# Kernel tuning notes

Measured on AMD Instinct MI355X. Metric: run time of the kernel, lower is better.

Reference implementation:

```python
import jax, jax.numpy as jnp
import numpy as np

OUT_SIZE = (7, 7, 7)
SPATIAL_SCALE = 1.0
SAMPLING_RATIO = 2
ALIGNED = True


def setup_inputs() -> dict:
    key = jax.random.key(0)
    kf, kc1, kc2 = jax.random.split(key, 3)
    B, C, D, H, W = 2, 128, 16, 64, 64
    N = 64
    features = jax.random.normal(kf, (B, C, D, H, W), dtype=jnp.float32)
    # Build valid boxes (z1,y1,x1,z2,y2,x2) inside the feature volume.
    dims = jnp.array([D, H, W], dtype=jnp.float32)
    lo = jax.random.uniform(kc1, (B, N, 3)) * dims * 0.6
    ext = 2.0 + jax.random.uniform(kc2, (B, N, 3)) * dims * 0.35
    hi = jnp.minimum(lo + ext, dims - 1.0)
    rois = jnp.concatenate([lo, hi], axis=-1).astype(jnp.float32)  # [B,N,6]
    return {"features": features, "rois": rois}


def _trilinear_sample(feat, z, y, x):
    # feat: [C,D,H,W]; z,y,x: [N,Pd,Ph,Pw] pixel coords (align_corners=False,
    # zero padding: out-of-bounds corners contribute 0).
    C, D, H, W = feat.shape
    z0f, y0f, x0f = jnp.floor(z), jnp.floor(y), jnp.floor(x)
    lz, ly, lx = z - z0f, y - y0f, x - x0f
    z0 = z0f.astype(jnp.int32)
    y0 = y0f.astype(jnp.int32)
    x0 = x0f.astype(jnp.int32)
    feat_flat = feat.reshape(C, -1)  # [C, D*H*W]

    def corner(zi, yi, xi, w):
        valid = ((zi >= 0) & (zi < D) & (yi >= 0) & (yi < H) & (xi >= 0) & (xi < W))
        idx = (jnp.clip(zi, 0, D - 1) * H + jnp.clip(yi, 0, H - 1)) * W + jnp.clip(xi, 0, W - 1)
        vals = jnp.take(feat_flat, idx.reshape(-1), axis=1).reshape((C,) + idx.shape)
        return vals * (w * valid.astype(w.dtype))[None]

    out = corner(z0, y0, x0, (1 - lz) * (1 - ly) * (1 - lx))
    out = out + corner(z0, y0, x0 + 1, (1 - lz) * (1 - ly) * lx)
    out = out + corner(z0, y0 + 1, x0, (1 - lz) * ly * (1 - lx))
    out = out + corner(z0, y0 + 1, x0 + 1, (1 - lz) * ly * lx)
    out = out + corner(z0 + 1, y0, x0, lz * (1 - ly) * (1 - lx))
    out = out + corner(z0 + 1, y0, x0 + 1, lz * (1 - ly) * lx)
    out = out + corner(z0 + 1, y0 + 1, x0, lz * ly * (1 - lx))
    out = out + corner(z0 + 1, y0 + 1, x0 + 1, lz * ly * lx)
    return out  # [C,N,Pd,Ph,Pw]


def _roi_align_3d(features, rois):
    B, C, D, H, W = features.shape
    od, oh, ow = OUT_SIZE
    s = SAMPLING_RATIO if SAMPLING_RATIO > 0 else 1
    dt = features.dtype
    d_step = (jnp.arange(od * s, dtype=dt) + 0.5) / s
    h_step = (jnp.arange(oh * s, dtype=dt) + 0.5) / s
    w_step = (jnp.arange(ow * s, dtype=dt) + 0.5) / s

    def per_batch(feat, roi):  # feat [C,D,H,W], roi [N,6]
        roi = roi * SPATIAL_SCALE
        if ALIGNED:
            roi = roi - 0.5
        z1, y1, x1, z2, y2, x2 = (roi[:, i] for i in range(6))
        bd = jnp.maximum(z2 - z1, 1e-6) / od
        bh = jnp.maximum(y2 - y1, 1e-6) / oh
        bw = jnp.maximum(x2 - x1, 1e-6) / ow
        zg = z1[:, None] + d_step[None, :] * bd[:, None]  # [N, od*s]
        yg = y1[:, None] + h_step[None, :] * bh[:, None]  # [N, oh*s]
        xg = x1[:, None] + w_step[None, :] * bw[:, None]  # [N, ow*s]
        z, y, x = jnp.broadcast_arrays(zg[:, :, None, None], yg[:, None, :, None], xg[:, None, None, :])
        sam = _trilinear_sample(feat, z, y, x)  # [C,N,od*s,oh*s,ow*s]
        N = roi.shape[0]
        sam = sam.reshape(C, N, od, s, oh, s, ow, s).mean(axis=(3, 5, 7))
        return sam.transpose(1, 0, 2, 3, 4)  # [N,C,od,oh,ow]

    return jax.vmap(per_batch)(features, rois)  # [B,N,C,od,oh,ow]


def reference(features, rois):
    return _roi_align_3d(features, rois)
```

## Files before the change

### kernel.cpp

```cpp
#include <hip/hip_runtime.h>

constexpr int Bc = 2, Nc = 64, Cc = 128, Dc = 16, Hc = 64, Wc = 64;
constexpr int OD = 7, OH = 7, OW = 7;
constexpr int CELLS = OD * OH * OW;
constexpr int DHW = Dc * Hc * Wc, HW = Hc * Wc;
constexpr int MAXZ = 10, MAXY = 25, MAXX = 25;
constexpr int SUBSZ = MAXZ * MAXY * (MAXX + 1);

typedef __fp16 h2 __attribute__((ext_vector_type(2)));

__device__ inline unsigned pk_f16(float a, float b) {
    return __builtin_bit_cast(unsigned, __builtin_amdgcn_cvt_pkrtz(a, b));
}

__device__ inline float fdot2(unsigned a, unsigned b, float c) {
#if __has_builtin(__builtin_amdgcn_fdot2)
    return __builtin_amdgcn_fdot2(__builtin_bit_cast(h2, a),
                                  __builtin_bit_cast(h2, b), c, false);
#else
    h2 ha = __builtin_bit_cast(h2, a);
    h2 hb = __builtin_bit_cast(h2, b);
    return fmaf((float)ha.x, (float)hb.x, fmaf((float)ha.y, (float)hb.y, c));
#endif
}

__global__ __launch_bounds__(384) void roialign3d_v11(
    const float* __restrict__ feat, const float* __restrict__ rois,
    float* __restrict__ out)
{
    __shared__ unsigned sub[SUBSZ + 2];
    __shared__ int2     tzp[14], typ[14];
    __shared__ float2   wzp[14], wyp[14];
    __shared__ int      txo[14];
    __shared__ unsigned wxh[14];

    const int blk = blockIdx.x;
    const int cp  = blk & 63;
    const int n   = (blk >> 6) & 63;
    const int b   = blk >> 12;
    const int tid = threadIdx.x;

    const float* rp = rois + (size_t)(b * Nc + n) * 6;
    float r1a[3] = {rp[0] - 0.5f, rp[1] - 0.5f, rp[2] - 0.5f};
    float r2a[3] = {rp[3] - 0.5f, rp[4] - 0.5f, rp[5] - 0.5f};
    const int dims[3] = {Dc, Hc, Wc};
    const int maxn[3] = {MAXZ, MAXY, MAXX};

    float bs[3]; int lo[3], ncnt[3];
    #pragma unroll
    for (int a = 0; a < 3; ++a) {
        bs[a] = fmaxf(r2a[a] - r1a[a], 1e-6f) * (1.0f / 7.0f);
        float smin = r1a[a] + 0.25f * bs[a];
        float smax = r1a[a] + 6.75f * bs[a];
        int l = max(0, (int)floorf(smin));
        int h = min(dims[a] - 1, (int)floorf(smax) + 1);
        lo[a] = l;
        ncnt[a] = min(h - l + 1, maxn[a]);
    }
    const int zn = ncnt[0], yn = ncnt[1], xn = ncnt[2];
    const int xnp = xn | 1;
    const int rows = zn * yn;
    const int zstride = yn * xnp;

    if (tid < 42) {
        int a = tid / 14, m = tid - a * 14;
        float v = r1a[a] + ((float)m + 0.5f) * 0.5f * bs[a];
        float f = floorf(v);
        float l = v - f;
        int i0 = (int)f;
        int d  = dims[a];
        float w0 = (i0 >= 0 && i0 < d) ? 1.0f - l : 0.0f;
        float w1 = (i0 + 1 < d) ? l : 0.0f;
        if (a == 0) {
            int c0 = min(max(i0 - lo[0], 0), zn - 1);
            int c1 = min(max(i0 + 1 - lo[0], 0), zn - 1);
            tzp[m] = make_int2(c0, c1);
            wzp[m] = make_float2(w0, w1);
        } else if (a == 1) {
            int c0 = min(max(i0 - lo[1], 0), yn - 1);
            int c1 = min(max(i0 + 1 - lo[1], 0), yn - 1);
            typ[m] = make_int2(c0 * xnp, c1 * xnp);
            wyp[m] = make_float2(w0, w1);
        } else {
            int c0 = min(max(i0 - lo[2], -1), xn - 1);
            txo[m] = c0;
            wxh[m] = pk_f16(w0, w1);
        }
    }
    if (tid == 64) sub[0] = 0;
    if (tid == 65) sub[1 + rows * xnp] = 0;

    const int c0ch = cp * 2;
    const float* fb = feat + ((size_t)b * Cc + c0ch) * DHW;
    const unsigned m32x = 0xFFFFFFFFu / (unsigned)xnp + 1u;
    const unsigned m32y = 0xFFFFFFFFu / (unsigned)yn + 1u;
    const int gz = lo[0] * HW + lo[1] * Wc + lo[2];
    const int total = rows * xnp;
    for (int p = tid; p < total; p += 384) {
        int row = (int)__umulhi((unsigned)p, m32x);
        int x   = p - row * xnp;
        int xs  = min(x, xn - 1);
        int z   = (int)__umulhi((unsigned)row, m32y);
        int y   = row - z * yn;
        int g   = gz + (z << 12) + (y << 6) + xs;
        sub[1 + p] = pk_f16(fb[g], fb[g + DHW]);
    }
    __syncthreads();

    if (tid < CELLS) {
        int i   = tid / 49;
        int rem = tid - i * 49;
        int j   = rem / 7;
        int k   = rem - j * 7;
        int4   tzr = *(const int4*)&tzp[2 * i];
        float4 wzv = *(const float4*)&wzp[2 * i];
        int4   ty  = *(const int4*)&typ[2 * j];
        float4 wyv = *(const float4*)&wyp[2 * j];
        int    xo0 = txo[2 * k], xo1 = txo[2 * k + 1];
        unsigned wh0 = wxh[2 * k], wh1 = wxh[2 * k + 1];

        const unsigned* G = sub + 1;

        int c0z = tzr.x;
        int p1 = tzr.y - c0z;
        int p2 = tzr.z - c0z;
        int p3 = tzr.w - c0z;
        float cz0 = wzv.x + (p1 == 0 ? wzv.y : 0.0f)
                  + (p2 == 0 ? wzv.z : 0.0f) + (p3 == 0 ? wzv.w : 0.0f);
        float cz1 = (p1 == 1 ? wzv.y : 0.0f)
                  + (p2 == 1 ? wzv.z : 0.0f) + (p3 == 1 ? wzv.w : 0.0f);
        float cz2 = (p3 == 2 ? wzv.w : 0.0f);
        int zb0 = c0z * zstride;
        int zb1 = min(c0z + 1, zn - 1) * zstride;
        int zb2 = min(c0z + 2, zn - 1) * zstride;

        const int   zbs[3] = {zb0, zb1, zb2};
        const float czs[3] = {cz0, cz1, cz2};
        const int   yo[4] = {ty.x, ty.y, ty.z, ty.w};
        const float wy[4] = {wyv.x, wyv.y, wyv.z, wyv.w};

        float a0 = 0.0f, a1 = 0.0f;
        #pragma unroll
        for (int d = 0; d < 3; ++d) {
            int zb = zbs[d];
            float s0 = 0.0f, s1 = 0.0f;
            #pragma unroll
            for (int yi = 0; yi < 4; ++yi) {
                int base = zb + yo[yi];
                unsigned p0a = G[base + xo0], p0b = G[base + xo0 + 1];
                unsigned p1a = G[base + xo1], p1b = G[base + xo1 + 1];
                unsigned c0p0 = __builtin_amdgcn_perm(p0b, p0a, 0x05040100u);
                unsigned c1p0 = __builtin_amdgcn_perm(p0b, p0a, 0x07060302u);
                unsigned c0p1 = __builtin_amdgcn_perm(p1b, p1a, 0x05040100u);
                unsigned c1p1 = __builtin_amdgcn_perm(p1b, p1a, 0x07060302u);
                float r0 = fdot2(c0p1, wh1, fdot2(c0p0, wh0, 0.0f));
                float r1 = fdot2(c1p1, wh1, fdot2(c1p0, wh0, 0.0f));
                s0 = fmaf(wy[yi], r0, s0);
                s1 = fmaf(wy[yi], r1, s1);
            }
            a0 = fmaf(czs[d], s0, a0);
            a1 = fmaf(czs[d], s1, a1);
        }
        size_t obase = ((size_t)(b * Nc + n) * Cc + c0ch) * CELLS;
        out[obase + tid]         = a0 * 0.125f;
        out[obase + CELLS + tid] = a1 * 0.125f;
    }
}

extern "C" void kernel_launch(void* const* d_in, const int* in_sizes, int n_in,
                              void* d_out, int out_size, void* d_ws, size_t ws_size,
                              hipStream_t stream) {
    const float* feat = (const float*)d_in[0];
    const float* rois = (const float*)d_in[1];
    float* out = (float*)d_out;
    int blocks = Bc * Nc * (Cc / 2);
    hipLaunchKernelGGL(roialign3d_v11, dim3(blocks), dim3(384), 0, stream,
                       feat, rois, out);
}
```

Baseline: 42.91 us.

## Precompute per-ROI tables in a prep kernel and use packed fp16 interpolation

Adds a small pre-kernel that computes each ROI's bounds, magic divisors and sample index/weight tables once and writes them to workspace. The main kernel then copies these tables into shared memory instead of recomputing them in every block. The inner trilinear loop now uses packed half2 multiply-adds, including the y accumulation, in place of perm plus fdot2 with fp32 accumulation. This trims redundant per-block setup and instruction count, at the cost of a second kernel launch and reduced accuracy from fp16 accumulation.

```diff
diff --git a/kernel.cpp b/kernel.cpp
--- a/kernel.cpp
+++ b/kernel.cpp
@@ -6,46 +6,27 @@
 constexpr int DHW = Dc * Hc * Wc, HW = Hc * Wc;
 constexpr int MAXZ = 10, MAXY = 25, MAXX = 25;
 constexpr int SUBSZ = MAXZ * MAXY * (MAXX + 1);
+constexpr int BLOB = 176;
+constexpr int TZP = 0, WZP = 28, TYP = 56, WYB = 84, WXB = 112, TXO = 140;
+constexpr int TBLN = 154;
 
-typedef __fp16 h2 __attribute__((ext_vector_type(2)));
+typedef _Float16 h2f __attribute__((ext_vector_type(2)));
 
 __device__ inline unsigned pk_f16(float a, float b) {
     return __builtin_bit_cast(unsigned, __builtin_amdgcn_cvt_pkrtz(a, b));
 }
+__device__ inline h2f uh(unsigned u) { return __builtin_bit_cast(h2f, u); }
 
-__device__ inline float fdot2(unsigned a, unsigned b, float c) {
-#if __has_builtin(__builtin_amdgcn_fdot2)
-    return __builtin_amdgcn_fdot2(__builtin_bit_cast(h2, a),
-                                  __builtin_bit_cast(h2, b), c, false);
-#else
-    h2 ha = __builtin_bit_cast(h2, a);
-    h2 hb = __builtin_bit_cast(h2, b);
-    return fmaf((float)ha.x, (float)hb.x, fmaf((float)ha.y, (float)hb.y, c));
-#endif
-}
-
-__global__ __launch_bounds__(384) void roialign3d_v11(
-    const float* __restrict__ feat, const float* __restrict__ rois,
-    float* __restrict__ out)
+__global__ __launch_bounds__(128) void roi_pre(
+    const float* __restrict__ rois, unsigned* __restrict__ ws)
 {
-    __shared__ unsigned sub[SUBSZ + 2];
-    __shared__ int2     tzp[14], typ[14];
-    __shared__ float2   wzp[14], wyp[14];
-    __shared__ int      txo[14];
-    __shared__ unsigned wxh[14];
-
-    const int blk = blockIdx.x;
-    const int cp  = blk & 63;
-    const int n   = (blk >> 6) & 63;
-    const int b   = blk >> 12;
-    const int tid = threadIdx.x;
-
-    const float* rp = rois + (size_t)(b * Nc + n) * 6;
+    int r = threadIdx.x;
+    if (r >= Bc * Nc) return;
+    const float* rp = rois + r * 6;
     float r1a[3] = {rp[0] - 0.5f, rp[1] - 0.5f, rp[2] - 0.5f};
     float r2a[3] = {rp[3] - 0.5f, rp[4] - 0.5f, rp[5] - 0.5f};
     const int dims[3] = {Dc, Hc, Wc};
     const int maxn[3] = {MAXZ, MAXY, MAXX};
-
     float bs[3]; int lo[3], ncnt[3];
     #pragma unroll
     for (int a = 0; a < 3; ++a) {
@@ -57,45 +38,85 @@
         lo[a] = l;
         ncnt[a] = min(h - l + 1, maxn[a]);
     }
-    const int zn = ncnt[0], yn = ncnt[1], xn = ncnt[2];
-    const int xnp = xn | 1;
-    const int rows = zn * yn;
-    const int zstride = yn * xnp;
+    int zn = ncnt[0], yn = ncnt[1], xn = ncnt[2];
+    int xnp = xn | 1;
+    int rows = zn * yn;
+    int total = rows * xnp;
+    int zstride = yn * xnp;
+    int gz = lo[0] * HW + lo[1] * Wc + lo[2];
+    unsigned m32x = 0xFFFFFFFFu / (unsigned)xnp + 1u;
+    unsigned m32y = 0xFFFFFFFFu / (unsigned)yn + 1u;
 
-    if (tid < 42) {
-        int a = tid / 14, m = tid - a * 14;
-        float v = r1a[a] + ((float)m + 0.5f) * 0.5f * bs[a];
-        float f = floorf(v);
-        float l = v - f;
-        int i0 = (int)f;
-        int d  = dims[a];
-        float w0 = (i0 >= 0 && i0 < d) ? 1.0f - l : 0.0f;
-        float w1 = (i0 + 1 < d) ? l : 0.0f;
-        if (a == 0) {
-            int c0 = min(max(i0 - lo[0], 0), zn - 1);
-            int c1 = min(max(i0 + 1 - lo[0], 0), zn - 1);
-            tzp[m] = make_int2(c0, c1);
-            wzp[m] = make_float2(w0, w1);
-        } else if (a == 1) {
-            int c0 = min(max(i0 - lo[1], 0), yn - 1);
-            int c1 = min(max(i0 + 1 - lo[1], 0), yn - 1);
-            typ[m] = make_int2(c0 * xnp, c1 * xnp);
-            wyp[m] = make_float2(w0, w1);
-        } else {
-            int c0 = min(max(i0 - lo[2], -1), xn - 1);
-            txo[m] = c0;
-            wxh[m] = pk_f16(w0, w1);
+    unsigned* blob = ws + r * BLOB;
+    blob[0] = (unsigned)total; blob[1] = (unsigned)xnp; blob[2] = (unsigned)xn;
+    blob[3] = (unsigned)yn;    blob[4] = (unsigned)gz;  blob[5] = m32x;
+    blob[6] = m32y;            blob[7] = (unsigned)zn;  blob[8] = (unsigned)zstride;
+    blob[9] = 0;
+    unsigned* tb = blob + 10;
+    for (int m = 0; m < 14; ++m) {
+        #pragma unroll
+        for (int a = 0; a < 3; ++a) {
+            float v = r1a[a] + ((float)m + 0.5f) * 0.5f * bs[a];
+            float f = floorf(v);
+            float l = v - f;
+            int i0 = (int)f;
+            int d  = dims[a];
+            float w0 = (i0 >= 0 && i0 < d) ? 1.0f - l : 0.0f;
+            float w1 = (i0 + 1 < d) ? l : 0.0f;
+            if (a == 0) {
+                int c0 = min(max(i0 - lo[0], 0), zn - 1);
+                int c1 = min(max(i0 + 1 - lo[0], 0), zn - 1);
+                tb[TZP + 2 * m]     = (unsigned)c0;
+                tb[TZP + 2 * m + 1] = (unsigned)c1;
+                ((float*)tb)[WZP + 2 * m]     = w0;
+                ((float*)tb)[WZP + 2 * m + 1] = w1;
+            } else if (a == 1) {
+                int c0 = min(max(i0 - lo[1], 0), yn - 1);
+                int c1 = min(max(i0 + 1 - lo[1], 0), yn - 1);
+                tb[TYP + 2 * m]     = (unsigned)(c0 * xnp);
+                tb[TYP + 2 * m + 1] = (unsigned)(c1 * xnp);
+                tb[WYB + 2 * m]     = pk_f16(w0, w0);
+                tb[WYB + 2 * m + 1] = pk_f16(w1, w1);
+            } else {
+                int c0 = min(max(i0 - lo[2], -1), xn - 1);
+                tb[TXO + m] = (unsigned)c0;
+                tb[WXB + 2 * m]     = pk_f16(w0, w0);
+                tb[WXB + 2 * m + 1] = pk_f16(w1, w1);
+            }
         }
     }
-    if (tid == 64) sub[0] = 0;
-    if (tid == 65) sub[1 + rows * xnp] = 0;
+}
+
+__global__ __launch_bounds__(384) void roialign3d_v12(
+    const float* __restrict__ feat, const unsigned* __restrict__ ws,
+    float* __restrict__ out)
+{
+    __shared__ __align__(16) unsigned sub[SUBSZ + 2];
+    __shared__ __align__(16) unsigned tbl[TBLN];
+
+    const int blk = blockIdx.x;
+    const int cp  = blk & 63;
+    const int n   = (blk >> 6) & 63;
+    const int b   = blk >> 12;
+    const int tid = threadIdx.x;
+
+    const unsigned* blob = ws + (unsigned)(b * Nc + n) * BLOB;
+    const int total   = (int)blob[0];
+    const int xnp     = (int)blob[1];
+    const int xn      = (int)blob[2];
+    const int yn      = (int)blob[3];
+    const int gz      = (int)blob[4];
+    const unsigned m32x = blob[5];
+    const unsigned m32y = blob[6];
+    const int zn      = (int)blob[7];
+    const int zstride = (int)blob[8];
+
+    if (tid < TBLN) tbl[tid] = blob[10 + tid];
+    if (tid == 352) sub[0] = 0;
+    if (tid == 353) sub[1 + total] = 0;
 
     const int c0ch = cp * 2;
     const float* fb = feat + ((size_t)b * Cc + c0ch) * DHW;
-    const unsigned m32x = 0xFFFFFFFFu / (unsigned)xnp + 1u;
-    const unsigned m32y = 0xFFFFFFFFu / (unsigned)yn + 1u;
-    const int gz = lo[0] * HW + lo[1] * Wc + lo[2];
-    const int total = rows * xnp;
     for (int p = tid; p < total; p += 384) {
         int row = (int)__umulhi((unsigned)p, m32x);
         int x   = p - row * xnp;
@@ -112,19 +133,20 @@
         int rem = tid - i * 49;
         int j   = rem / 7;
         int k   = rem - j * 7;
-        int4   tzr = *(const int4*)&tzp[2 * i];
-        float4 wzv = *(const float4*)&wzp[2 * i];
-        int4   ty  = *(const int4*)&typ[2 * j];
-        float4 wyv = *(const float4*)&wyp[2 * j];
-        int    xo0 = txo[2 * k], xo1 = txo[2 * k + 1];
-        unsigned wh0 = wxh[2 * k], wh1 = wxh[2 * k + 1];
+        int4   tzr = *(const int4*)&tbl[TZP + 4 * i];
+        float4 wzv = *(const float4*)&tbl[WZP + 4 * i];
+        int4   ty  = *(const int4*)&tbl[TYP + 4 * j];
+        uint4  wyb = *(const uint4*)&tbl[WYB + 4 * j];
+        uint4  wxb = *(const uint4*)&tbl[WXB + 4 * k];
+        int xo0 = (int)tbl[TXO + 2 * k], xo1 = (int)tbl[TXO + 2 * k + 1];
 
         const unsigned* G = sub + 1;
+        h2f wx00 = uh(wxb.x), wx01 = uh(wxb.y);
+        h2f wx10 = uh(wxb.z), wx11 = uh(wxb.w);
+        const h2f wys[4] = {uh(wyb.x), uh(wyb.y), uh(wyb.z), uh(wyb.w)};
 
         int c0z = tzr.x;
-        int p1 = tzr.y - c0z;
-        int p2 = tzr.z - c0z;
-        int p3 = tzr.w - c0z;
+        int p1 = tzr.y - c0z, p2 = tzr.z - c0z, p3 = tzr.w - c0z;
         float cz0 = wzv.x + (p1 == 0 ? wzv.y : 0.0f)
                   + (p2 == 0 ? wzv.z : 0.0f) + (p3 == 0 ? wzv.w : 0.0f);
         float cz1 = (p1 == 1 ? wzv.y : 0.0f)
@@ -136,30 +158,23 @@
 
         const int   zbs[3] = {zb0, zb1, zb2};
         const float czs[3] = {cz0, cz1, cz2};
-        const int   yo[4] = {ty.x, ty.y, ty.z, ty.w};
-        const float wy[4] = {wyv.x, wyv.y, wyv.z, wyv.w};
+        const int   yo[4]  = {ty.x, ty.y, ty.z, ty.w};
 
         float a0 = 0.0f, a1 = 0.0f;
         #pragma unroll
         for (int d = 0; d < 3; ++d) {
             int zb = zbs[d];
-            float s0 = 0.0f, s1 = 0.0f;
+            h2f s = {(_Float16)0, (_Float16)0};
             #pragma unroll
             for (int yi = 0; yi < 4; ++yi) {
                 int base = zb + yo[yi];
-                unsigned p0a = G[base + xo0], p0b = G[base + xo0 + 1];
-                unsigned p1a = G[base + xo1], p1b = G[base + xo1 + 1];
-                unsigned c0p0 = __builtin_amdgcn_perm(p0b, p0a, 0x05040100u);
-                unsigned c1p0 = __builtin_amdgcn_perm(p0b, p0a, 0x07060302u);
-                unsigned c0p1 = __builtin_amdgcn_perm(p1b, p1a, 0x05040100u);
-                unsigned c1p1 = __builtin_amdgcn_perm(p1b, p1a, 0x07060302u);
-                float r0 = fdot2(c0p1, wh1, fdot2(c0p0, wh0, 0.0f));
-                float r1 = fdot2(c1p1, wh1, fdot2(c1p0, wh0, 0.0f));
-                s0 = fmaf(wy[yi], r0, s0);
-                s1 = fmaf(wy[yi], r1, s1);
+                h2f A0 = uh(G[base + xo0]), A1 = uh(G[base + xo0 + 1]);
+                h2f B0 = uh(G[base + xo1]), B1 = uh(G[base + xo1 + 1]);
+                h2f xr = A0 * wx00 + A1 * wx01 + B0 * wx10 + B1 * wx11;
+                s = s + wys[yi] * xr;
             }
-            a0 = fmaf(czs[d], s0, a0);
-            a1 = fmaf(czs[d], s1, a1);
+            a0 = fmaf(czs[d], (float)s.x, a0);
+            a1 = fmaf(czs[d], (float)s.y, a1);
         }
         size_t obase = ((size_t)(b * Nc + n) * Cc + c0ch) * CELLS;
         out[obase + tid]         = a0 * 0.125f;
@@ -173,7 +188,8 @@
     const float* feat = (const float*)d_in[0];
     const float* rois = (const float*)d_in[1];
     float* out = (float*)d_out;
-    int blocks = Bc * Nc * (Cc / 2);
-    hipLaunchKernelGGL(roialign3d_v11, dim3(blocks), dim3(384), 0, stream,
-                       feat, rois, out);
+    unsigned* ws = (unsigned*)d_ws;
+    hipLaunchKernelGGL(roi_pre, dim3(1), dim3(128), 0, stream, rois, ws);
+    hipLaunchKernelGGL(roialign3d_v12, dim3(Bc * Nc * (Cc / 2)), dim3(384), 0,
+                       stream, feat, (const unsigned*)ws, out);
 }
```

After: 44.09 us. 1.03x slower.
